# Performance work log

Hardware: AMD Instinct MI355X
Metric: run time of the kernel (lower is better)

## Reference

```python
import jax, jax.numpy as jnp
import numpy as np

BATCH = 2
SEQ = 2048
D_MODEL = 512
D_STATE = 16
D_CONV = 4
D_INNER = 2 * D_MODEL  # expand=2


def setup_inputs() -> dict:
    key = jax.random.key(0)
    ks = jax.random.split(key, 7)
    s = 0.02
    x = jax.random.normal(ks[0], (BATCH, SEQ, D_MODEL), jnp.float32)
    W_in = jax.random.normal(ks[1], (2 * D_INNER, D_MODEL), jnp.float32) * s
    conv_w = jax.random.normal(ks[2], (D_INNER, 1, D_CONV), jnp.float32) * s  # depthwise kernel
    conv_b = jnp.zeros((D_INNER,), jnp.float32)
    W_x = jax.random.normal(ks[3], (2 * D_STATE, D_INNER), jnp.float32) * s
    W_dt = jax.random.normal(ks[4], (D_INNER, D_INNER), jnp.float32) * s
    b_dt = jnp.zeros((D_INNER,), jnp.float32)
    # A_log init: log of [1..d_state] broadcast over d_inner rows
    A_log = jnp.log(jnp.broadcast_to(jnp.arange(1, D_STATE + 1, dtype=jnp.float32), (D_INNER, D_STATE)))
    D_param = jnp.ones((D_INNER,), jnp.float32)
    W_out = jax.random.normal(ks[5], (D_MODEL, D_INNER), jnp.float32) * s
    return dict(x=x, W_in=W_in, conv_w=conv_w, conv_b=conv_b, W_x=W_x,
                W_dt=W_dt, b_dt=b_dt, A_log=A_log, D_param=D_param, W_out=W_out)


def reference(x, W_in, conv_w, conv_b, W_x, W_dt, b_dt, A_log, D_param, W_out):
    # in_proj, split into x-branch and gate z
    xz = x @ W_in.T                             # [B, L, 2*di]
    xi, z = jnp.split(xz, 2, axis=-1)
    # depthwise causal conv1d (torch pads both sides then slices [:seq_len] == left-pad only)
    h = jnp.transpose(xi, (0, 2, 1))            # [B, di, L]
    h = jax.lax.conv_general_dilated(
        h, conv_w, window_strides=(1,), padding=[(D_CONV - 1, 0)],
        dimension_numbers=('NCH', 'OIH', 'NCH'), feature_group_count=D_INNER)
    h = h + conv_b[None, :, None]
    h = jax.nn.silu(jnp.transpose(h, (0, 2, 1)))  # [B, L, di]

    A = -jnp.exp(A_log)                         # [di, ds]
    x_dbl = h @ W_x.T                           # [B, L, 2*ds]
    _delta_unused, Bmat = jnp.split(x_dbl, 2, axis=-1)  # B (also used as C): [B, L, ds]
    delta = jax.nn.softplus(h @ W_dt.T + b_dt)  # [B, L, di] (overwrites x_proj delta, as in source)

    def step(state, inp):
        d_t, B_t, h_t = inp                     # [B,di], [B,ds], [B,di]
        dA = jnp.exp(d_t[:, :, None] * A)       # [B, di, ds]
        state = dA * state + d_t[:, :, None] * B_t[:, None, :] * h_t[:, :, None]
        y_t = jnp.einsum('bds,bs->bd', state, B_t)  # C == B
        return state, y_t

    init = jnp.zeros((x.shape[0], D_INNER, D_STATE), x.dtype)
    _, ys = jax.lax.scan(step, init,
                         (jnp.swapaxes(delta, 0, 1), jnp.swapaxes(Bmat, 0, 1), jnp.swapaxes(h, 0, 1)))
    y = jnp.swapaxes(ys, 0, 1)                  # [B, L, di]
    y = (y + D_param * h) * jax.nn.silu(z)
    return y @ W_out.T                          # [B, L, d_model]
```

## Files before the change

### kernel.cpp

```cpp
#include <hip/hip_runtime.h>
#include <cstddef>
#include <cstdint>

#define NB 2
#define L_SEQ 2048
#define DM 512
#define DS 16
#define DI 1024
#define NC 64
#define CL (L_SEQ/NC)

typedef __attribute__((ext_vector_type(4))) float f32x4;
typedef __attribute__((ext_vector_type(8))) short bf16x8;

__device__ __forceinline__ float softplus_f(float x) {
  return (x > 20.f) ? x : log1pf(expf(x));
}
__device__ __forceinline__ float silu_f(float x) {
  return x / (1.f + expf(-x));
}
__device__ __forceinline__ ushort f2bf(float f) {
  uint32_t u = __float_as_uint(f);
  return (ushort)((u + 0x7fffu + ((u >> 16) & 1u)) >> 16);
}
__device__ __forceinline__ float bf2f(ushort h) {
  return __uint_as_float(((uint32_t)h) << 16);
}

__device__ __forceinline__ void gload16(const void* g, ushort* lds_wave_base) {
  __builtin_amdgcn_global_load_lds(
      (const __attribute__((address_space(1))) void*)g,
      (__attribute__((address_space(3))) void*)lds_wave_base, 16, 0, 0);
}

__global__ __launch_bounds__(256) void split_bf16(
    const float* __restrict__ in, ushort* __restrict__ hi,
    ushort* __restrict__ lo, int n4) {
  int i = blockIdx.x * 256 + threadIdx.x;
  if (i >= n4) return;
  float4 v = ((const float4*)in)[i];
  ushort h0 = f2bf(v.x), h1 = f2bf(v.y), h2 = f2bf(v.z), h3 = f2bf(v.w);
  ((ushort4*)hi)[i] = make_ushort4(h0, h1, h2, h3);
  ((ushort4*)lo)[i] = make_ushort4(
      f2bf(v.x - bf2f(h0)), f2bf(v.y - bf2f(h1)),
      f2bf(v.z - bf2f(h2)), f2bf(v.w - bf2f(h3)));
}

template <int BN, int ACT>
__global__ __launch_bounds__(256, 2) void gemm_mfma(
    const ushort* __restrict__ Ahi, const ushort* __restrict__ Alo, int lda,
    const ushort* __restrict__ Bhi, const ushort* __restrict__ Blo, int ldb,
    const float* __restrict__ bias, float* __restrict__ C, int ldc, int K) {
  constexpr int BM = 128;
  constexpr int AT = BM * 32;
  constexpr int BT = BN * 32;
  constexpr int BUF = 2 * AT + 2 * BT;
  constexpr int MR = 4, NR = BN / 32;
  __shared__ __align__(16) ushort lds[2 * BUF];

  const int tid = threadIdx.x;
  const int lane = tid & 63;
  const int wave = tid >> 6;
  const int wr = wave >> 1, wc = wave & 1;

  const int nx = gridDim.x;
  const int nwg = nx * gridDim.y;
  int bid = blockIdx.y * nx + blockIdx.x;
  bid = (bid & 7) * (nwg >> 3) + (bid >> 3);
  const int m0 = (bid / nx) * BM;
  const int n0 = (bid % nx) * BN;

  const int r0 = tid >> 2;
  const int kg = (tid & 3) ^ ((r0 >> 1) & 3);
  const size_t aoff0 = (size_t)(m0 + r0) * lda + kg * 8;
  const size_t aoff1 = (size_t)(m0 + r0 + 64) * lda + kg * 8;
  const size_t boff0 = (size_t)(n0 + r0) * ldb + kg * 8;
  const size_t boff1 = (size_t)(n0 + r0 + 64) * ldb + kg * 8;

  const int fr = lane & 15, fq = lane >> 4;
  const int kswz = fq ^ ((fr >> 1) & 3);
  int aoffs[MR], boffs[NR];
#pragma unroll
  for (int m = 0; m < MR; m++) aoffs[m] = (wr * 64 + m * 16 + fr) * 32 + kswz * 8;
#pragma unroll
  for (int n = 0; n < NR; n++) boffs[n] = (wc * (BN / 2) + n * 16 + fr) * 32 + kswz * 8;

  f32x4 acc[MR][NR];
#pragma unroll
  for (int m = 0; m < MR; m++)
#pragma unroll
    for (int n = 0; n < NR; n++) acc[m][n] = (f32x4){0.f, 0.f, 0.f, 0.f};

  const int nsteps = K >> 5;

#define STAGE(bufi, kk)                                              \
  {                                                                  \
    ushort* base = lds + (bufi) * BUF;                               \
    gload16(Ahi + aoff0 + (kk), base + wave * 512);                  \
    gload16(Ahi + aoff1 + (kk), base + 2048 + wave * 512);           \
    gload16(Alo + aoff0 + (kk), base + AT + wave * 512);             \
    gload16(Alo + aoff1 + (kk), base + AT + 2048 + wave * 512);      \
    gload16(Bhi + boff0 + (kk), base + 2 * AT + wave * 512);         \
    gload16(Blo + boff0 + (kk), base + 2 * AT + BT + wave * 512);    \
    if (BN == 128) {                                                 \
      gload16(Bhi + boff1 + (kk), base + 2 * AT + 2048 + wave * 512);\
      gload16(Blo + boff1 + (kk), base + 2 * AT + BT + 2048 + wave * 512);\
    }                                                                \
  }

#define COMPUTE(bufi)                                                          \
  {                                                                            \
    const ushort* base = lds + (bufi) * BUF;                                   \
    bf16x8 ah[MR], al[MR], bh[NR], bl[NR];                                     \
    _Pragma("unroll")                                                          \
    for (int m = 0; m < MR; m++) ah[m] = *(const bf16x8*)(base + aoffs[m]);    \
    _Pragma("unroll")                                                          \
    for (int m = 0; m < MR; m++) al[m] = *(const bf16x8*)(base + AT + aoffs[m]);\
    _Pragma("unroll")                                                          \
    for (int n = 0; n < NR; n++) bh[n] = *(const bf16x8*)(base + 2 * AT + boffs[n]);\
    _Pragma("unroll")                                                          \
    for (int n = 0; n < NR; n++) bl[n] = *(const bf16x8*)(base + 2 * AT + BT + boffs[n]);\
    _Pragma("unroll")                                                          \
    for (int m = 0; m < MR; m++)                                               \
      _Pragma("unroll")                                                        \
      for (int n = 0; n < NR; n++)                                             \
        acc[m][n] = __builtin_amdgcn_mfma_f32_16x16x32_bf16(ah[m], bh[n], acc[m][n], 0, 0, 0);\
    _Pragma("unroll")                                                          \
    for (int m = 0; m < MR; m++)                                               \
      _Pragma("unroll")                                                        \
      for (int n = 0; n < NR; n++)                                             \
        acc[m][n] = __builtin_amdgcn_mfma_f32_16x16x32_bf16(al[m], bh[n], acc[m][n], 0, 0, 0);\
    _Pragma("unroll")                                                          \
    for (int m = 0; m < MR; m++)                                               \
      _Pragma("unroll")                                                        \
      for (int n = 0; n < NR; n++)                                             \
        acc[m][n] = __builtin_amdgcn_mfma_f32_16x16x32_bf16(ah[m], bl[n], acc[m][n], 0, 0, 0);\
  }

  STAGE(0, 0);
  __syncthreads();
  for (int t = 0; t < nsteps - 1; ++t) {
    STAGE((t + 1) & 1, (t + 1) << 5);
    COMPUTE(t & 1);
    __syncthreads();
  }
  COMPUTE((nsteps - 1) & 1);
#undef STAGE
#undef COMPUTE

#pragma unroll
  for (int m = 0; m < MR; m++) {
    const int row = m0 + wr * 64 + m * 16 + fq * 4;
#pragma unroll
    for (int n = 0; n < NR; n++) {
      const int col = n0 + wc * (BN / 2) + n * 16 + fr;
      float bcol = (ACT == 1) ? bias[col] : 0.f;
#pragma unroll
      for (int j = 0; j < 4; j++) {
        float v = acc[m][n][j];
        if (ACT == 1) v = softplus_f(v + bcol);
        C[(size_t)(row + j) * ldc + col] = v;
      }
    }
  }
}

__global__ __launch_bounds__(256) void conv_silu_kernel(
    const float* __restrict__ xz, const float* __restrict__ conv_w,
    const float* __restrict__ conv_b, float* __restrict__ h,
    ushort* __restrict__ h_hi, ushort* __restrict__ h_lo) {
  const int idx = blockIdx.x * 256 + threadIdx.x;
  const int c = idx & (DI - 1);
  const int r = idx >> 10;
  const int l = r & (L_SEQ - 1);
  const float w0 = conv_w[c * 4 + 0];
  const float w1 = conv_w[c * 4 + 1];
  const float w2 = conv_w[c * 4 + 2];
  const float w3 = conv_w[c * 4 + 3];
  const float* xp = xz + (size_t)r * (2 * DI) + c;
  float acc = conv_b[c];
  if (l >= 3) acc += xp[-3 * 2 * DI] * w0;
  if (l >= 2) acc += xp[-2 * 2 * DI] * w1;
  if (l >= 1) acc += xp[-1 * 2 * DI] * w2;
  acc += xp[0] * w3;
  const float hv = silu_f(acc);
  h[idx] = hv;
  const ushort hh = f2bf(hv);
  h_hi[idx] = hh;
  h_lo[idx] = f2bf(hv - bf2f(hh));
}

__global__ __launch_bounds__(256) void xproj_kernel(
    const float* __restrict__ h, const float* __restrict__ W_x,
    float* __restrict__ Bm) {
  const int idx = blockIdx.x * 256 + threadIdx.x;
  const int s = idx & 15;
  const int r = idx >> 4;
  const float* hp = h + (size_t)r * DI;
  const float* wp = W_x + (size_t)(DS + s) * DI;
  float acc = 0.f;
  for (int k = 0; k < DI; k += 4) {
    float4 hv = *(const float4*)(hp + k);
    float4 wv = *(const float4*)(wp + k);
    acc += hv.x * wv.x + hv.y * wv.y + hv.z * wv.z + hv.w * wv.w;
  }
  Bm[idx] = acc;
}

__global__ __launch_bounds__(256) void scan_phase1(
    const float* __restrict__ delta, const float* __restrict__ h,
    const float* __restrict__ Bm, const float* __restrict__ A_log,
    float* __restrict__ aprod, float* __restrict__ blocal) {
  __shared__ float sB[CL * DS];
  const int tid = threadIdx.x;
  const int bid = blockIdx.x;
  const int cblk = bid & 3;
  const int chunk = (bid >> 2) & (NC - 1);
  const int b = bid >> 8;
  const int c = cblk * 256 + tid;
  const size_t row0 = (size_t)b * L_SEQ + chunk * CL;
  ((float2*)sB)[tid] = ((const float2*)(Bm + row0 * DS))[tid];
  __syncthreads();

  float Acs[DS], state[DS];
#pragma unroll
  for (int s = 0; s < DS; s += 4) {
    float4 al = *(const float4*)(A_log + (size_t)c * DS + s);
    Acs[s + 0] = -__expf(al.x);
    Acs[s + 1] = -__expf(al.y);
    Acs[s + 2] = -__expf(al.z);
    Acs[s + 3] = -__expf(al.w);
    state[s + 0] = 0.f; state[s + 1] = 0.f; state[s + 2] = 0.f; state[s + 3] = 0.f;
  }
  const float* dp = delta + row0 * DI + c;
  const float* hp = h + row0 * DI + c;
  float sdt = 0.f;
  for (int t = 0; t < CL; ++t) {
    const float dt = dp[(size_t)t * DI];
    const float ht = hp[(size_t)t * DI];
    const float dth = dt * ht;
    sdt += dt;
#pragma unroll
    for (int s = 0; s < DS; ++s)
      state[s] = __expf(dt * Acs[s]) * state[s] + dth * sB[t * DS + s];
  }
  const size_t o = (((size_t)b * NC + chunk) * DI + c) * DS;
#pragma unroll
  for (int s = 0; s < DS; s += 4) {
    *(float4*)(aprod + o + s) = make_float4(
        __expf(Acs[s] * sdt), __expf(Acs[s + 1] * sdt),
        __expf(Acs[s + 2] * sdt), __expf(Acs[s + 3] * sdt));
    *(float4*)(blocal + o + s) = make_float4(state[s], state[s + 1], state[s + 2], state[s + 3]);
  }
}

__global__ __launch_bounds__(256) void scan_phase2(
    float* __restrict__ aprod, const float* __restrict__ blocal) {
  const int idx = blockIdx.x * 256 + threadIdx.x;
  const int b = idx >> 14;
  const int cs = idx & 16383;
  float st = 0.f;
  for (int ch = 0; ch < NC; ++ch) {
    const size_t o = (size_t)(b * NC + ch) * (DI * DS) + cs;
    const float a = aprod[o];
    const float bl = blocal[o];
    aprod[o] = st;
    st = a * st + bl;
  }
}

__global__ __launch_bounds__(256) void scan_phase3(
    const float* __restrict__ delta, const float* __restrict__ h,
    const float* __restrict__ Bm, const float* __restrict__ A_log,
    const float* __restrict__ sinit, float* __restrict__ xz,
    const float* __restrict__ Dp) {
  __shared__ float sB[CL * DS];
  const int tid = threadIdx.x;
  const int bid = blockIdx.x;
  const int cblk = bid & 3;
  const int chunk = (bid >> 2) & (NC - 1);
  const int b = bid >> 8;
  const int c = cblk * 256 + tid;
  const size_t row0 = (size_t)b * L_SEQ + chunk * CL;
  ((float2*)sB)[tid] = ((const float2*)(Bm + row0 * DS))[tid];
  __syncthreads();

  float Acs[DS], state[DS];
  const size_t o = (((size_t)b * NC + chunk) * DI + c) * DS;
#pragma unroll
  for (int s = 0; s < DS; s += 4) {
    float4 al = *(const float4*)(A_log + (size_t)c * DS + s);
    Acs[s + 0] = -__expf(al.x);
    Acs[s + 1] = -__expf(al.y);
    Acs[s + 2] = -__expf(al.z);
    Acs[s + 3] = -__expf(al.w);
    float4 sv = *(const float4*)(sinit + o + s);
    state[s + 0] = sv.x; state[s + 1] = sv.y; state[s + 2] = sv.z; state[s + 3] = sv.w;
  }
  const float* dp = delta + row0 * DI + c;
  const float* hp = h + row0 * DI + c;
  const float* zp = xz + row0 * (2 * DI) + DI + c;
  ushort* yrow = (ushort*)(xz + row0 * (2 * DI)) + c;
  const float Dc = Dp[c];
  for (int t = 0; t < CL; ++t) {
    const float dt = dp[(size_t)t * DI];
    const float ht = hp[(size_t)t * DI];
    const float z = zp[(size_t)t * (2 * DI)];
    const float dth = dt * ht;
    float yv = 0.f;
#pragma unroll
    for (int s = 0; s < DS; ++s) {
      const float bt = sB[t * DS + s];
      state[s] = __expf(dt * Acs[s]) * state[s] + dth * bt;
      yv += state[s] * bt;
    }
    const float g = (yv + Dc * ht) * silu_f(z);
    const ushort gh = f2bf(g);
    yrow[(size_t)t * 4096] = gh;
    yrow[(size_t)t * 4096 + 1024] = f2bf(g - bf2f(gh));
  }
}

extern "C" void kernel_launch(void* const* d_in, const int* in_sizes, int n_in,
                              void* d_out, int out_size, void* d_ws, size_t ws_size,
                              hipStream_t stream) {
  const float* x      = (const float*)d_in[0];
  const float* W_in   = (const float*)d_in[1];
  const float* conv_w = (const float*)d_in[2];
  const float* conv_b = (const float*)d_in[3];
  const float* W_x    = (const float*)d_in[4];
  const float* W_dt   = (const float*)d_in[5];
  const float* b_dt   = (const float*)d_in[6];
  const float* A_log  = (const float*)d_in[7];
  const float* D_par  = (const float*)d_in[8];
  const float* W_out  = (const float*)d_in[9];
  float* out = (float*)d_out;

  const int rows = NB * L_SEQ;

  float* xz     = (float*)d_ws;
  float* h      = xz + (size_t)(8u << 20);
  float* delta  = h + (size_t)(4u << 20);
  float* Bm     = delta + (size_t)(4u << 20);
  float* spare  = Bm + (size_t)(64u << 10);
  float* wreg   = spare + (size_t)((3u << 20) / 2);
  ushort* Wdt_hi  = (ushort*)wreg;
  ushort* Wdt_lo  = Wdt_hi + (size_t)(1u << 20);
  ushort* Wout_hi = Wdt_lo + (size_t)(1u << 20);
  ushort* Wout_lo = Wout_hi + (size_t)(512u << 10);
  float* xreg   = wreg + (size_t)((3u << 20) / 2);
  ushort* x_hi  = (ushort*)xreg;
  ushort* x_lo  = x_hi + (size_t)(2u << 20);
  ushort* Win_hi = x_lo + (size_t)(2u << 20);
  ushort* Win_lo = Win_hi + (size_t)(1u << 20);
  ushort* h_hi  = (ushort*)xreg;
  ushort* h_lo  = h_hi + (size_t)(4u << 20);
  float* aprod  = xreg;
  float* blocal = aprod + (size_t)(2u << 20);
  ushort* y_hi  = (ushort*)xz;
  ushort* y_lo  = y_hi + 1024;

  split_bf16<<<2048, 256, 0, stream>>>(x, x_hi, x_lo, rows * DM / 4);
  split_bf16<<<1024, 256, 0, stream>>>(W_in, Win_hi, Win_lo, 2 * DI * DM / 4);
  split_bf16<<<1024, 256, 0, stream>>>(W_dt, Wdt_hi, Wdt_lo, DI * DI / 4);
  split_bf16<<<512, 256, 0, stream>>>(W_out, Wout_hi, Wout_lo, DM * DI / 4);

  gemm_mfma<128, 0><<<dim3(16, 32), 256, 0, stream>>>(
      x_hi, x_lo, DM, Win_hi, Win_lo, DM, nullptr, xz, 2 * DI, DM);
  conv_silu_kernel<<<(rows * DI) / 256, 256, 0, stream>>>(xz, conv_w, conv_b, h, h_hi, h_lo);
  gemm_mfma<64, 1><<<dim3(16, 32), 256, 0, stream>>>(
      h_hi, h_lo, DI, Wdt_hi, Wdt_lo, DI, b_dt, delta, DI, DI);
  xproj_kernel<<<(rows * DS) / 256, 256, 0, stream>>>(h, W_x, Bm);
  scan_phase1<<<NB * NC * (DI / 256), 256, 0, stream>>>(delta, h, Bm, A_log, aprod, blocal);
  scan_phase2<<<(NB * DI * DS) / 256, 256, 0, stream>>>(aprod, blocal);
  scan_phase3<<<NB * NC * (DI / 256), 256, 0, stream>>>(delta, h, Bm, A_log, aprod, xz, D_par);
  gemm_mfma<64, 0><<<dim3(8, 32), 256, 0, stream>>>(
      y_hi, y_lo, 4096, Wout_hi, Wout_lo, DI, nullptr, out, DM, DI);
}
```

Baseline: 231.7 us.

## Triple-buffer GEMM LDS loads with vmcnt waits and retile GEMM blocks

The bf16x3 MFMA GEMM switches from a double-buffered loop with full __syncthreads to a three-stage LDS ring, prefetching two k-steps ahead. It waits with explicit s_waitcnt vmcnt counts plus s_barrier, so loads stay in flight across iterations. BM becomes a template parameter: the in_proj GEMM moves from 128x128 to 128x64 tiles and the out_proj GEMM to 64x64 tiles, both increasing the grid size. The trade-off is more LDS per block and the removal of the 2-blocks-per-CU launch bound, which may reduce occupancy.

```diff
diff --git a/kernel.cpp b/kernel.cpp
--- a/kernel.cpp
+++ b/kernel.cpp
@@ -31,6 +31,14 @@
   __builtin_amdgcn_global_load_lds(
       (const __attribute__((address_space(1))) void*)g,
       (__attribute__((address_space(3))) void*)lds_wave_base, 16, 0, 0);
+}
+
+template <int N>
+__device__ __forceinline__ void wait_vm() {
+  if constexpr (N == 0)      asm volatile("s_waitcnt vmcnt(0)" ::: "memory");
+  else if constexpr (N == 4) asm volatile("s_waitcnt vmcnt(4)" ::: "memory");
+  else if constexpr (N == 6) asm volatile("s_waitcnt vmcnt(6)" ::: "memory");
+  else if constexpr (N == 8) asm volatile("s_waitcnt vmcnt(8)" ::: "memory");
 }
 
 __global__ __launch_bounds__(256) void split_bf16(
@@ -46,17 +54,17 @@
       f2bf(v.z - bf2f(h2)), f2bf(v.w - bf2f(h3)));
 }
 
-template <int BN, int ACT>
-__global__ __launch_bounds__(256, 2) void gemm_mfma(
+template <int BM, int BN, int ACT>
+__global__ __launch_bounds__(256) void gemm_mfma(
     const ushort* __restrict__ Ahi, const ushort* __restrict__ Alo, int lda,
     const ushort* __restrict__ Bhi, const ushort* __restrict__ Blo, int ldb,
     const float* __restrict__ bias, float* __restrict__ C, int ldc, int K) {
-  constexpr int BM = 128;
   constexpr int AT = BM * 32;
   constexpr int BT = BN * 32;
   constexpr int BUF = 2 * AT + 2 * BT;
-  constexpr int MR = 4, NR = BN / 32;
-  __shared__ __align__(16) ushort lds[2 * BUF];
+  constexpr int MR = BM / 32, NR = BN / 32;
+  constexpr int LPS = (BM / 64) * 2 + (BN / 64) * 2;
+  __shared__ __align__(16) ushort lds[3 * BUF];
 
   const int tid = threadIdx.x;
   const int lane = tid & 63;
@@ -75,13 +83,12 @@
   const size_t aoff0 = (size_t)(m0 + r0) * lda + kg * 8;
   const size_t aoff1 = (size_t)(m0 + r0 + 64) * lda + kg * 8;
   const size_t boff0 = (size_t)(n0 + r0) * ldb + kg * 8;
-  const size_t boff1 = (size_t)(n0 + r0 + 64) * ldb + kg * 8;
 
   const int fr = lane & 15, fq = lane >> 4;
   const int kswz = fq ^ ((fr >> 1) & 3);
   int aoffs[MR], boffs[NR];
 #pragma unroll
-  for (int m = 0; m < MR; m++) aoffs[m] = (wr * 64 + m * 16 + fr) * 32 + kswz * 8;
+  for (int m = 0; m < MR; m++) aoffs[m] = (wr * (BM / 2) + m * 16 + fr) * 32 + kswz * 8;
 #pragma unroll
   for (int n = 0; n < NR; n++) boffs[n] = (wc * (BN / 2) + n * 16 + fr) * 32 + kswz * 8;
 
@@ -93,64 +100,62 @@
 
   const int nsteps = K >> 5;
 
-#define STAGE(bufi, kk)                                              \
-  {                                                                  \
-    ushort* base = lds + (bufi) * BUF;                               \
-    gload16(Ahi + aoff0 + (kk), base + wave * 512);                  \
-    gload16(Ahi + aoff1 + (kk), base + 2048 + wave * 512);           \
-    gload16(Alo + aoff0 + (kk), base + AT + wave * 512);             \
-    gload16(Alo + aoff1 + (kk), base + AT + 2048 + wave * 512);      \
-    gload16(Bhi + boff0 + (kk), base + 2 * AT + wave * 512);         \
-    gload16(Blo + boff0 + (kk), base + 2 * AT + BT + wave * 512);    \
-    if (BN == 128) {                                                 \
-      gload16(Bhi + boff1 + (kk), base + 2 * AT + 2048 + wave * 512);\
-      gload16(Blo + boff1 + (kk), base + 2 * AT + BT + 2048 + wave * 512);\
-    }                                                                \
-  }
-
-#define COMPUTE(bufi)                                                          \
+#define STAGE(base, kk)                                                     \
+  {                                                                         \
+    ushort* bp = (base);                                                    \
+    gload16(Ahi + aoff0 + (kk), bp + wave * 512);                           \
+    if constexpr (BM == 128) gload16(Ahi + aoff1 + (kk), bp + 2048 + wave * 512); \
+    gload16(Alo + aoff0 + (kk), bp + AT + wave * 512);                      \
+    if constexpr (BM == 128) gload16(Alo + aoff1 + (kk), bp + AT + 2048 + wave * 512); \
+    gload16(Bhi + boff0 + (kk), bp + 2 * AT + wave * 512);                  \
+    gload16(Blo + boff0 + (kk), bp + 2 * AT + BT + wave * 512);             \
+  }
+
+#define COMPUTE(base)                                                          \
   {                                                                            \
-    const ushort* base = lds + (bufi) * BUF;                                   \
+    const ushort* cp = (base);                                                 \
     bf16x8 ah[MR], al[MR], bh[NR], bl[NR];                                     \
     _Pragma("unroll")                                                          \
-    for (int m = 0; m < MR; m++) ah[m] = *(const bf16x8*)(base + aoffs[m]);    \
-    _Pragma("unroll")                                                          \
-    for (int m = 0; m < MR; m++) al[m] = *(const bf16x8*)(base + AT + aoffs[m]);\
-    _Pragma("unroll")                                                          \
-    for (int n = 0; n < NR; n++) bh[n] = *(const bf16x8*)(base + 2 * AT + boffs[n]);\
-    _Pragma("unroll")                                                          \
-    for (int n = 0; n < NR; n++) bl[n] = *(const bf16x8*)(base + 2 * AT + BT + boffs[n]);\
+    for (int m = 0; m < MR; m++) ah[m] = *(const bf16x8*)(cp + aoffs[m]);      \
+    _Pragma("unroll")                                                          \
+    for (int m = 0; m < MR; m++) al[m] = *(const bf16x8*)(cp + AT + aoffs[m]); \
+    _Pragma("unroll")                                                          \
+    for (int n = 0; n < NR; n++) bh[n] = *(const bf16x8*)(cp + 2 * AT + boffs[n]); \
+    _Pragma("unroll")                                                          \
+    for (int n = 0; n < NR; n++) bl[n] = *(const bf16x8*)(cp + 2 * AT + BT + boffs[n]); \
     _Pragma("unroll")                                                          \
     for (int m = 0; m < MR; m++)                                               \
       _Pragma("unroll")                                                        \
       for (int n = 0; n < NR; n++)                                             \
-        acc[m][n] = __builtin_amdgcn_mfma_f32_16x16x32_bf16(ah[m], bh[n], acc[m][n], 0, 0, 0);\
+        acc[m][n] = __builtin_amdgcn_mfma_f32_16x16x32_bf16(ah[m], bh[n], acc[m][n], 0, 0, 0); \
     _Pragma("unroll")                                                          \
     for (int m = 0; m < MR; m++)                                               \
       _Pragma("unroll")                                                        \
       for (int n = 0; n < NR; n++)                                             \
-        acc[m][n] = __builtin_amdgcn_mfma_f32_16x16x32_bf16(al[m], bh[n], acc[m][n], 0, 0, 0);\
+        acc[m][n] = __builtin_amdgcn_mfma_f32_16x16x32_bf16(al[m], bh[n], acc[m][n], 0, 0, 0); \
     _Pragma("unroll")                                                          \
     for (int m = 0; m < MR; m++)                                               \
       _Pragma("unroll")                                                        \
       for (int n = 0; n < NR; n++)                                             \
-        acc[m][n] = __builtin_amdgcn_mfma_f32_16x16x32_bf16(ah[m], bl[n], acc[m][n], 0, 0, 0);\
-  }
-
-  STAGE(0, 0);
-  __syncthreads();
-  for (int t = 0; t < nsteps - 1; ++t) {
-    STAGE((t + 1) & 1, (t + 1) << 5);
-    COMPUTE(t & 1);
-    __syncthreads();
-  }
-  COMPUTE((nsteps - 1) & 1);
+        acc[m][n] = __builtin_amdgcn_mfma_f32_16x16x32_bf16(ah[m], bl[n], acc[m][n], 0, 0, 0); \
+  }
+
+  STAGE(lds, 0);
+  STAGE(lds + BUF, 32);
+  int ocur = 0, onext = BUF, ofar = 2 * BUF;
+  for (int t = 0; t < nsteps; ++t) {
+    if (t == nsteps - 1) wait_vm<0>(); else wait_vm<LPS>();
+    __builtin_amdgcn_s_barrier();
+    if (t + 2 < nsteps) STAGE(lds + ofar, (t + 2) << 5);
+    COMPUTE(lds + ocur);
+    int tmp = ocur; ocur = onext; onext = ofar; ofar = tmp;
+  }
 #undef STAGE
 #undef COMPUTE
 
 #pragma unroll
   for (int m = 0; m < MR; m++) {
-    const int row = m0 + wr * 64 + m * 16 + fq * 4;
+    const int row = m0 + wr * (BM / 2) + m * 16 + fq * 4;
 #pragma unroll
     for (int n = 0; n < NR; n++) {
       const int col = n0 + wc * (BN / 2) + n * 16 + fr;
@@ -365,15 +370,15 @@
   split_bf16<<<1024, 256, 0, stream>>>(W_dt, Wdt_hi, Wdt_lo, DI * DI / 4);
   split_bf16<<<512, 256, 0, stream>>>(W_out, Wout_hi, Wout_lo, DM * DI / 4);
 
-  gemm_mfma<128, 0><<<dim3(16, 32), 256, 0, stream>>>(
+  gemm_mfma<128, 64, 0><<<dim3(32, 32), 256, 0, stream>>>(
       x_hi, x_lo, DM, Win_hi, Win_lo, DM, nullptr, xz, 2 * DI, DM);
   conv_silu_kernel<<<(rows * DI) / 256, 256, 0, stream>>>(xz, conv_w, conv_b, h, h_hi, h_lo);
-  gemm_mfma<64, 1><<<dim3(16, 32), 256, 0, stream>>>(
+  gemm_mfma<128, 64, 1><<<dim3(16, 32), 256, 0, stream>>>(
       h_hi, h_lo, DI, Wdt_hi, Wdt_lo, DI, b_dt, delta, DI, DI);
   xproj_kernel<<<(rows * DS) / 256, 256, 0, stream>>>(h, W_x, Bm);
   scan_phase1<<<NB * NC * (DI / 256), 256, 0, stream>>>(delta, h, Bm, A_log, aprod, blocal);
   scan_phase2<<<(NB * DI * DS) / 256, 256, 0, stream>>>(aprod, blocal);
   scan_phase3<<<NB * NC * (DI / 256), 256, 0, stream>>>(delta, h, Bm, A_log, aprod, xz, D_par);
-  gemm_mfma<64, 0><<<dim3(8, 32), 256, 0, stream>>>(
+  gemm_mfma<64, 64, 0><<<dim3(8, 64), 256, 0, stream>>>(
       y_hi, y_lo, 4096, Wout_hi, Wout_lo, DI, nullptr, out, DM, DI);
 }
```

Result: no change. 230.6 us (-0.5%).

## Restructure MFMA GEMM to stage only A in LDS and read B directly from global

Applied to the files above, without the earlier changes.

Rewrites the split-bf16 GEMM kernel to 512 threads, each wave covering 32 rows. Only the A tile goes through LDS; B fragments are loaded straight from global memory into registers. The double-buffered LDS pipeline is replaced by a single buffer with two barriers per k-step, and tile widths and grids change for all three projections. The aim is less LDS traffic and higher occupancy, at the cost of losing load/compute overlap and issuing uncoalesced global reads for B.

```diff
diff --git a/kernel.cpp b/kernel.cpp
--- a/kernel.cpp
+++ b/kernel.cpp
@@ -47,21 +47,20 @@
 }
 
 template <int BN, int ACT>
-__global__ __launch_bounds__(256, 2) void gemm_mfma(
+__global__ __launch_bounds__(512, 4) void gemm_bd(
     const ushort* __restrict__ Ahi, const ushort* __restrict__ Alo, int lda,
     const ushort* __restrict__ Bhi, const ushort* __restrict__ Blo, int ldb,
     const float* __restrict__ bias, float* __restrict__ C, int ldc, int K) {
   constexpr int BM = 128;
-  constexpr int AT = BM * 32;
-  constexpr int BT = BN * 32;
-  constexpr int BUF = 2 * AT + 2 * BT;
-  constexpr int MR = 4, NR = BN / 32;
-  __shared__ __align__(16) ushort lds[2 * BUF];
+  constexpr int MR = 2;
+  constexpr int NR = BN / 32;
+  __shared__ __align__(16) ushort As[2 * BM * 32];
 
   const int tid = threadIdx.x;
   const int lane = tid & 63;
   const int wave = tid >> 6;
-  const int wr = wave >> 1, wc = wave & 1;
+  const int wr = wave >> 1;
+  const int wc = wave & 1;
 
   const int nx = gridDim.x;
   const int nwg = nx * gridDim.y;
@@ -70,20 +69,22 @@
   const int m0 = (bid / nx) * BM;
   const int n0 = (bid % nx) * BN;
 
-  const int r0 = tid >> 2;
-  const int kg = (tid & 3) ^ ((r0 >> 1) & 3);
-  const size_t aoff0 = (size_t)(m0 + r0) * lda + kg * 8;
-  const size_t aoff1 = (size_t)(m0 + r0 + 64) * lda + kg * 8;
-  const size_t boff0 = (size_t)(n0 + r0) * ldb + kg * 8;
-  const size_t boff1 = (size_t)(n0 + r0 + 64) * ldb + kg * 8;
+  const int ra = tid >> 2;
+  const int kga = (tid & 3) ^ (ra & 3);
+  const size_t aoff = (size_t)(m0 + ra) * lda + kga * 8;
+  ushort* aldsh = As + wave * 512;
+  ushort* aldsl = As + 4096 + wave * 512;
 
   const int fr = lane & 15, fq = lane >> 4;
-  const int kswz = fq ^ ((fr >> 1) & 3);
-  int aoffs[MR], boffs[NR];
-#pragma unroll
-  for (int m = 0; m < MR; m++) aoffs[m] = (wr * 64 + m * 16 + fr) * 32 + kswz * 8;
-#pragma unroll
-  for (int n = 0; n < NR; n++) boffs[n] = (wc * (BN / 2) + n * 16 + fr) * 32 + kswz * 8;
+  const int kswz = fq ^ (fr & 3);
+  int aoffs[MR];
+#pragma unroll
+  for (int m = 0; m < MR; m++) aoffs[m] = (wr * 32 + m * 16 + fr) * 32 + kswz * 8;
+
+  size_t boffs[NR];
+#pragma unroll
+  for (int n = 0; n < NR; n++)
+    boffs[n] = (size_t)(n0 + wc * (BN / 2) + n * 16 + fr) * ldb + fq * 8;
 
   f32x4 acc[MR][NR];
 #pragma unroll
@@ -92,65 +93,43 @@
     for (int n = 0; n < NR; n++) acc[m][n] = (f32x4){0.f, 0.f, 0.f, 0.f};
 
   const int nsteps = K >> 5;
-
-#define STAGE(bufi, kk)                                              \
-  {                                                                  \
-    ushort* base = lds + (bufi) * BUF;                               \
-    gload16(Ahi + aoff0 + (kk), base + wave * 512);                  \
-    gload16(Ahi + aoff1 + (kk), base + 2048 + wave * 512);           \
-    gload16(Alo + aoff0 + (kk), base + AT + wave * 512);             \
-    gload16(Alo + aoff1 + (kk), base + AT + 2048 + wave * 512);      \
-    gload16(Bhi + boff0 + (kk), base + 2 * AT + wave * 512);         \
-    gload16(Blo + boff0 + (kk), base + 2 * AT + BT + wave * 512);    \
-    if (BN == 128) {                                                 \
-      gload16(Bhi + boff1 + (kk), base + 2 * AT + 2048 + wave * 512);\
-      gload16(Blo + boff1 + (kk), base + 2 * AT + BT + 2048 + wave * 512);\
-    }                                                                \
-  }
-
-#define COMPUTE(bufi)                                                          \
-  {                                                                            \
-    const ushort* base = lds + (bufi) * BUF;                                   \
-    bf16x8 ah[MR], al[MR], bh[NR], bl[NR];                                     \
-    _Pragma("unroll")                                                          \
-    for (int m = 0; m < MR; m++) ah[m] = *(const bf16x8*)(base + aoffs[m]);    \
-    _Pragma("unroll")                                                          \
-    for (int m = 0; m < MR; m++) al[m] = *(const bf16x8*)(base + AT + aoffs[m]);\
-    _Pragma("unroll")                                                          \
-    for (int n = 0; n < NR; n++) bh[n] = *(const bf16x8*)(base + 2 * AT + boffs[n]);\
-    _Pragma("unroll")                                                          \
-    for (int n = 0; n < NR; n++) bl[n] = *(const bf16x8*)(base + 2 * AT + BT + boffs[n]);\
-    _Pragma("unroll")                                                          \
-    for (int m = 0; m < MR; m++)                                               \
-      _Pragma("unroll")                                                        \
-      for (int n = 0; n < NR; n++)                                             \
-        acc[m][n] = __builtin_amdgcn_mfma_f32_16x16x32_bf16(ah[m], bh[n], acc[m][n], 0, 0, 0);\
-    _Pragma("unroll")                                                          \
-    for (int m = 0; m < MR; m++)                                               \
-      _Pragma("unroll")                                                        \
-      for (int n = 0; n < NR; n++)                                             \
-        acc[m][n] = __builtin_amdgcn_mfma_f32_16x16x32_bf16(al[m], bh[n], acc[m][n], 0, 0, 0);\
-    _Pragma("unroll")                                                          \
-    for (int m = 0; m < MR; m++)                                               \
-      _Pragma("unroll")                                                        \
-      for (int n = 0; n < NR; n++)                                             \
-        acc[m][n] = __builtin_amdgcn_mfma_f32_16x16x32_bf16(ah[m], bl[n], acc[m][n], 0, 0, 0);\
-  }
-
-  STAGE(0, 0);
-  __syncthreads();
-  for (int t = 0; t < nsteps - 1; ++t) {
-    STAGE((t + 1) & 1, (t + 1) << 5);
-    COMPUTE(t & 1);
+  for (int t = 0; t < nsteps; ++t) {
+    const int kk = t << 5;
     __syncthreads();
-  }
-  COMPUTE((nsteps - 1) & 1);
-#undef STAGE
-#undef COMPUTE
+    gload16(Ahi + aoff + kk, aldsh);
+    gload16(Alo + aoff + kk, aldsl);
+    __syncthreads();
+    bf16x8 ah[MR], al[MR], bh[NR], bl[NR];
+#pragma unroll
+    for (int n = 0; n < NR; n++) {
+      bh[n] = *(const bf16x8*)(Bhi + boffs[n] + kk);
+      bl[n] = *(const bf16x8*)(Blo + boffs[n] + kk);
+    }
+#pragma unroll
+    for (int m = 0; m < MR; m++) {
+      ah[m] = *(const bf16x8*)(As + aoffs[m]);
+      al[m] = *(const bf16x8*)(As + 4096 + aoffs[m]);
+    }
+#pragma unroll
+    for (int m = 0; m < MR; m++)
+#pragma unroll
+      for (int n = 0; n < NR; n++)
+        acc[m][n] = __builtin_amdgcn_mfma_f32_16x16x32_bf16(ah[m], bh[n], acc[m][n], 0, 0, 0);
+#pragma unroll
+    for (int m = 0; m < MR; m++)
+#pragma unroll
+      for (int n = 0; n < NR; n++)
+        acc[m][n] = __builtin_amdgcn_mfma_f32_16x16x32_bf16(al[m], bh[n], acc[m][n], 0, 0, 0);
+#pragma unroll
+    for (int m = 0; m < MR; m++)
+#pragma unroll
+      for (int n = 0; n < NR; n++)
+        acc[m][n] = __builtin_amdgcn_mfma_f32_16x16x32_bf16(ah[m], bl[n], acc[m][n], 0, 0, 0);
+  }
 
 #pragma unroll
   for (int m = 0; m < MR; m++) {
-    const int row = m0 + wr * 64 + m * 16 + fq * 4;
+    const int row = m0 + wr * 32 + m * 16 + fq * 4;
 #pragma unroll
     for (int n = 0; n < NR; n++) {
       const int col = n0 + wc * (BN / 2) + n * 16 + fr;
@@ -365,15 +344,15 @@
   split_bf16<<<1024, 256, 0, stream>>>(W_dt, Wdt_hi, Wdt_lo, DI * DI / 4);
   split_bf16<<<512, 256, 0, stream>>>(W_out, Wout_hi, Wout_lo, DM * DI / 4);
 
-  gemm_mfma<128, 0><<<dim3(16, 32), 256, 0, stream>>>(
+  gemm_bd<64, 0><<<dim3(32, 32), 512, 0, stream>>>(
       x_hi, x_lo, DM, Win_hi, Win_lo, DM, nullptr, xz, 2 * DI, DM);
   conv_silu_kernel<<<(rows * DI) / 256, 256, 0, stream>>>(xz, conv_w, conv_b, h, h_hi, h_lo);
-  gemm_mfma<64, 1><<<dim3(16, 32), 256, 0, stream>>>(
+  gemm_bd<64, 1><<<dim3(16, 32), 512, 0, stream>>>(
       h_hi, h_lo, DI, Wdt_hi, Wdt_lo, DI, b_dt, delta, DI, DI);
   xproj_kernel<<<(rows * DS) / 256, 256, 0, stream>>>(h, W_x, Bm);
   scan_phase1<<<NB * NC * (DI / 256), 256, 0, stream>>>(delta, h, Bm, A_log, aprod, blocal);
   scan_phase2<<<(NB * DI * DS) / 256, 256, 0, stream>>>(aprod, blocal);
   scan_phase3<<<NB * NC * (DI / 256), 256, 0, stream>>>(delta, h, Bm, A_log, aprod, xz, D_par);
-  gemm_mfma<64, 0><<<dim3(8, 32), 256, 0, stream>>>(
+  gemm_bd<32, 0><<<dim3(16, 32), 512, 0, stream>>>(
       y_hi, y_lo, 4096, Wout_hi, Wout_lo, DI, nullptr, out, DM, DI);
 }
```

Measured after the change: 339.6 us. 1.47x slower.
